# Performance work log

Hardware: AMD Instinct MI355X
Metric: run time of the kernel (lower is better)

Reference implementation:

```python
import jax, jax.numpy as jnp
import numpy as np

EPS = 1e-7
CAPS_N = 1152   # 32 maps * 6 * 6
CAPS1_DIM = 8
CAPS2_N = 10
CAPS2_DIM = 16


def squash(s, axis):
    sq = jnp.sum(jnp.square(s), axis=axis, keepdims=True)
    norm = jnp.sqrt(sq + EPS)
    return (sq / (1.0 + sq)) * (s / norm)


def _conv(x, k, b, stride):
    y = jax.lax.conv_general_dilated(x, k, (stride, stride), 'VALID',
                                     dimension_numbers=('NHWC', 'HWIO', 'NHWC'))
    return jax.nn.relu(y + b)


def setup_inputs() -> dict:
    key = jax.random.key(0)
    ks = jax.random.split(key, 8)
    B = 256
    return {
        'image': jax.random.uniform(ks[0], (B, 28, 28, 1), dtype=jnp.float32),
        'target': jax.random.randint(ks[1], (B,), 0, CAPS2_N),
        'conv1_w': jax.random.normal(ks[2], (9, 9, 1, 256), jnp.float32) * 0.05,
        'conv1_b': jnp.zeros((256,), jnp.float32),
        'conv2_w': jax.random.normal(ks[3], (9, 9, 256, 256), jnp.float32) * 0.02,
        'conv2_b': jnp.zeros((256,), jnp.float32),
        'W': jax.random.normal(ks[4], (1, CAPS_N, CAPS2_N, CAPS2_DIM, CAPS1_DIM), jnp.float32) * 0.1,
        'd1_w': jax.random.normal(ks[5], (CAPS2_N * CAPS2_DIM, 512), jnp.float32) * 0.05,
        'd1_b': jnp.zeros((512,), jnp.float32),
        'd2_w': jax.random.normal(ks[6], (512, 1024), jnp.float32) * 0.04,
        'd2_b': jnp.zeros((1024,), jnp.float32),
        'd3_w': jax.random.normal(ks[7], (1024, 784), jnp.float32) * 0.03,
        'd3_b': jnp.zeros((784,), jnp.float32),
    }


def reference(image, target, conv1_w, conv1_b, conv2_w, conv2_b, W,
              d1_w, d1_b, d2_w, d2_b, d3_w, d3_b):
    B = image.shape[0]
    h = _conv(image, conv1_w, conv1_b, 1)        # [B,20,20,256]
    h = _conv(h, conv2_w, conv2_b, 2)            # [B,6,6,256]
    pc = squash(h.reshape(B, CAPS_N, CAPS1_DIM), axis=-1)  # [B,1152,8]
    # u_hat[b,n,c,j] = sum_i W[0,n,c,j,i] * pc[b,n,i]  (avoids explicit tiling)
    u_hat = jnp.einsum('ncji,bni->bncj', W[0], pc)          # [B,1152,10,16]
    # round 1: softmax of zeros over the 10 digit caps == uniform 1/10
    s1 = jnp.sum(u_hat, axis=1) * (1.0 / CAPS2_N)           # [B,10,16]
    v1 = squash(s1, axis=-1)
    # agreement uv[b,n,c] = <u_hat[b,n,c,:], v1[b,c,:]>
    uv = jnp.einsum('bncj,bcj->bnc', u_hat, v1)             # [B,1152,10]
    # round 2
    c2 = jax.nn.softmax(uv, axis=2)
    s2 = jnp.einsum('bnc,bncj->bcj', c2, u_hat)             # [B,10,16]
    v2 = squash(s2, axis=-1)                                # [B,10,16]
    norm_v2 = jnp.sqrt(jnp.sum(jnp.square(v2), axis=-1, keepdims=True) + EPS)
    norm_v2 = norm_v2[:, None, :, :, None]                  # [B,1,10,1,1]
    y_pred = jnp.squeeze(jnp.argmax(norm_v2, axis=2), axis=(1, 2))  # [B,1]
    # training path: mask by target one-hot
    mask = jax.nn.one_hot(target, CAPS2_N, dtype=v2.dtype)  # [B,10]
    masked = v2 * mask[:, :, None]                          # [B,10,16]
    flat = masked.reshape(B, 1, CAPS2_N * CAPS2_DIM)        # [B,1,160]
    h1 = jax.nn.relu(flat @ d1_w + d1_b)
    h2 = jax.nn.relu(h1 @ d2_w + d2_b)
    dec = jax.nn.sigmoid(h2 @ d3_w + d3_b)                  # [B,1,784]
    return norm_v2, y_pred, dec
```

## Files before the change

### kernel.cpp

```cpp
#include <hip/hip_runtime.h>
#include <math.h>

#define EPS 1e-7f
#define IN1_ELEMS 26214400
#define BT_ELEMS  5308416

typedef float fvec4 __attribute__((ext_vector_type(4)));
typedef short short8 __attribute__((ext_vector_type(8)));
typedef _Float16 half8 __attribute__((ext_vector_type(8)));

__device__ inline unsigned short f2h(float f){
  _Float16 h = (_Float16)f;
  return __builtin_bit_cast(unsigned short, h);
}
__device__ inline float h2f(unsigned short u){
  return (float)__builtin_bit_cast(_Float16, u);
}
__device__ inline void async16(unsigned short* dst, const unsigned short* src){
  __builtin_amdgcn_global_load_lds((const __attribute__((address_space(1))) void*)src,
                                   (__attribute__((address_space(3))) void*)dst, 16, 0, 0);
}
__device__ inline fvec4 mfma_f16(short8 a, short8 b, fvec4 c){
  return __builtin_amdgcn_mfma_f32_16x16x32_f16(
      __builtin_bit_cast(half8, a), __builtin_bit_cast(half8, b), c, 0, 0, 0);
}

__global__ __launch_bounds__(256) void prep_kernel(const float* __restrict__ w2,
    unsigned short* __restrict__ BTh, unsigned short* __restrict__ BTl,
    float* __restrict__ c2out,
    const float* __restrict__ img, const float* __restrict__ w1,
    const float* __restrict__ b1, unsigned short* __restrict__ outh,
    float* __restrict__ s1s2){
  const int bid = blockIdx.x;
  const int t = threadIdx.x;
  if (bid < 1296){
    __shared__ float tile[64][65];
    int k0 = (bid % 324) * 64, oc0 = (bid / 324) * 64;
    for (int g = bid*256 + t; g < 2359296; g += 1296*256) c2out[g] = 0.f;
    #pragma unroll
    for (int p = 0; p < 16; ++p){
      int f = p*256 + t;
      int kr = f >> 6, cc = f & 63;
      tile[kr][cc] = w2[(size_t)(k0 + kr)*256 + oc0 + cc];
    }
    __syncthreads();
    #pragma unroll
    for (int p = 0; p < 16; ++p){
      int f = p*256 + t;
      int ocr = f >> 6, kc = f & 63;
      float v = tile[kc][ocr] * 64.f;
      unsigned short h = f2h(v);
      size_t idx = (size_t)(oc0 + ocr)*20736 + k0 + kc;
      BTh[idx] = h;
      BTl[idx] = f2h(v - h2f(h));
    }
  } else {
    const int cid = bid - 1296;
    if (cid < 320) s1s2[cid*256 + t] = 0.f;
    __shared__ float sim[252];
    int oh = cid % 20, b = cid / 20;
    if (t < 252) sim[t] = img[((size_t)b*28 + oh + t/28)*28 + (t%28)];
    __syncthreads();
    float acc[20];
    #pragma unroll
    for (int i = 0; i < 20; ++i) acc[i] = 0.f;
    #pragma unroll
    for (int kh = 0; kh < 9; ++kh){
      float im[28];
      #pragma unroll
      for (int c = 0; c < 28; ++c) im[c] = sim[kh*28 + c];
      #pragma unroll
      for (int kw = 0; kw < 9; ++kw){
        float wv = w1[(kh*9 + kw)*256 + t];
        #pragma unroll
        for (int ow = 0; ow < 20; ++ow) acc[ow] = fmaf(im[ow + kw], wv, acc[ow]);
      }
    }
    float bv = b1[t];
    size_t base = ((size_t)(b*20 + oh))*20*256 + t;
    #pragma unroll
    for (int ow = 0; ow < 20; ++ow){
      float v = fmaxf(acc[ow] + bv, 0.f);
      outh[base + ow*256] = f2h(v * 0.015625f);
    }
  }
}

__global__ __launch_bounds__(256) void conv2_mfma(const unsigned short* __restrict__ in1h,
    const unsigned short* __restrict__ BTh, float* __restrict__ out){
  __shared__ __align__(16) unsigned short lds[24576];
  const int t = threadIdx.x;
  const int lane = t & 63, w = t >> 6;
  const int m0 = blockIdx.y * 128, n0 = blockIdx.x * 128;
  const int rowA = t >> 2, q = (t & 3) ^ ((t >> 3) & 3);

  const unsigned short* aS[2];
  const unsigned short* bS[2];
  #pragma unroll
  for (int h = 0; h < 2; ++h){
    int m = m0 + h*64 + rowA;
    int bb = m / 36, s = m - bb*36, oh = s / 6, ow = s - oh*6;
    aS[h] = in1h + ((size_t)((bb*20 + 2*oh)*20 + 2*ow))*256 + q*8;
    int n = n0 + h*64 + rowA;
    bS[h] = BTh + (size_t)n*20736 + q*8;
  }

  const int r = lane & 15;
  const int p = (lane >> 4) ^ ((lane >> 1) & 3);
  int roA[4], roB[4];
  #pragma unroll
  for (int i=0;i<4;++i){
    roA[i] = ((w >> 1)*64 + i*16 + r)*32 + p*8;
    roB[i] = ((w & 1)*64  + i*16 + r)*32 + p*8;
  }

  fvec4 acc[4][4];
  #pragma unroll
  for (int i=0;i<4;++i)
    #pragma unroll
    for (int j=0;j<4;++j) acc[i][j] = (fvec4){0.f,0.f,0.f,0.f};

  const int ks0 = blockIdx.z * 54;

  #define STAGE(BUF, KS) do{                                            \
    int kk_ = (KS) >> 3, kh_ = kk_/9, kw_ = kk_ - kh_*9;                \
    int aoff_ = (kh_*20 + kw_)*256 + ((KS) & 7)*32;                     \
    int boff_ = (KS)*32;                                                \
    int base_ = (BUF)*12288;                                            \
    _Pragma("unroll")                                                   \
    for (int h_=0; h_<2; ++h_){                                         \
      async16(&lds[base_ +        h_*2048 + t*8], aS[h_] + aoff_);      \
      async16(&lds[base_ + 4096 + h_*2048 + t*8], bS[h_] + boff_);      \
      async16(&lds[base_ + 8192 + h_*2048 + t*8], bS[h_] + BT_ELEMS + boff_); \
    } }while(0)

  STAGE(0, ks0);
  int buf = 0;
  for (int it = 0; it < 54; ++it){
    __syncthreads();
    if (it < 53) STAGE(buf^1, ks0 + it + 1);
    int base = buf*12288;
    short8 af[4], bh[4], bl[4];
    #pragma unroll
    for (int i=0;i<4;++i){
      af[i] = *(const short8*)&lds[base + roA[i]];
      bh[i] = *(const short8*)&lds[base + 4096 + roB[i]];
      bl[i] = *(const short8*)&lds[base + 8192 + roB[i]];
    }
    #pragma unroll
    for (int i=0;i<4;++i)
      #pragma unroll
      for (int j=0;j<4;++j){
        acc[i][j] = mfma_f16(af[i], bh[j], acc[i][j]);
        acc[i][j] = mfma_f16(af[i], bl[j], acc[i][j]);
      }
    buf ^= 1;
  }

  const int qm = (w >> 1)*64, qn = (w & 1)*64;
  #pragma unroll
  for (int i=0;i<4;++i){
    int gm = m0 + qm + i*16 + ((lane >> 4) << 2);
    #pragma unroll
    for (int j=0;j<4;++j){
      int gn = n0 + qn + j*16 + (lane & 15);
      #pragma unroll
      for (int rr=0;rr<4;++rr)
        atomicAdd(&out[(size_t)(gm + rr)*256 + gn], acc[i][j][rr]);
    }
  }
}

__global__ __launch_bounds__(256) void s1pc_kernel(const float* __restrict__ c2out,
    const float* __restrict__ b2, float* __restrict__ pc,
    const float* __restrict__ Wm, float* __restrict__ s1){
  __shared__ float pcl[2048];
  int t = threadIdx.x;
  int n0 = blockIdx.x * 16, b0 = blockIdx.y * 16;
  int pix = n0 >> 5, oc0 = (n0 & 31) * 8;
  {
    int bl = t >> 4, part = t & 15;
    const float* s = c2out + ((size_t)((b0 + bl)*36 + pix))*256 + oc0 + part*8;
    float v[8], sq = 0.f;
    #pragma unroll
    for (int e=0;e<8;++e){
      float x = fmaxf(s[e] + b2[oc0 + part*8 + e], 0.f);
      v[e] = x; sq += x*x;
    }
    float fac = sq / ((1.f + sq) * sqrtf(sq + EPS));
    float* o = pc + ((size_t)(b0 + bl)*1152 + n0 + part)*8;
    float* l = &pcl[(bl*16 + part)*8];
    #pragma unroll
    for (int e=0;e<8;++e){ float y = v[e]*fac; o[e] = y; l[e] = y; }
  }
  __syncthreads();
  for (int r = 0; r < 10; ++r){
    int item = r*256 + t;
    int bl = item / 160, cj = item - bl*160;
    float s1a = 0.f;
    const float* pb = &pcl[bl*128];
    #pragma unroll 4
    for (int nl = 0; nl < 16; ++nl){
      const float4* wp = (const float4*)&Wm[((size_t)(n0 + nl)*160 + cj)*8];
      float4 w0 = wp[0], w1 = wp[1];
      const float4* pp = (const float4*)&pb[nl*8];
      float4 p0 = pp[0], p1 = pp[1];
      s1a += w0.x*p0.x + w0.y*p0.y + w0.z*p0.z + w0.w*p0.w
           + w1.x*p1.x + w1.y*p1.y + w1.z*p1.z + w1.w*p1.w;
    }
    atomicAdd(&s1[(b0 + bl)*160 + cj], s1a);
  }
}

__global__ __launch_bounds__(320) void routing2(const float* __restrict__ pc,
    const float* __restrict__ Wm, const float* __restrict__ s1, float* __restrict__ s2){
  __shared__ float pcl[32][64];
  __shared__ float v1l[8][160];
  __shared__ float facl[80];
  __shared__ float c2l[32][10][8];
  const int t = threadIdx.x;
  const int n0 = blockIdx.x*32, b0 = blockIdx.y*8;

  for (int f = t; f < 2048; f += 320){
    int b = f >> 8, rem = f & 255;
    pcl[rem >> 3][b*8 + (rem & 7)] =
        pc[((size_t)(b0 + b)*1152 + n0 + (rem >> 3))*8 + (rem & 7)];
  }
  if (t < 80){
    int b = t/10, c = t - (t/10)*10;
    const float* s = s1 + (size_t)(b0 + b)*160 + c*16;
    float sq = 0.f;
    #pragma unroll
    for (int j=0;j<16;++j){ float v = s[j]*0.1f; sq += v*v; }
    facl[t] = 0.1f * sq / ((1.f + sq) * sqrtf(sq + EPS));
  }
  __syncthreads();
  for (int f = t; f < 1280; f += 320){
    int b = f / 160, cj = f - b*160;
    v1l[b][cj] = s1[(size_t)(b0 + b)*160 + cj] * facl[b*10 + (cj >> 4)];
  }
  __syncthreads();

  {
    const int nl = t / 10, c = t - (t/10)*10;
    float pcr[64];
    #pragma unroll
    for (int u = 0; u < 16; ++u) ((float4*)pcr)[u] = ((const float4*)&pcl[nl][0])[u];
    const float* wrow = Wm + ((size_t)(n0 + nl)*160 + c*16)*8;
    float uv[8];
    #pragma unroll
    for (int b=0;b<8;++b) uv[b] = 0.f;
    #pragma unroll
    for (int j = 0; j < 16; ++j){
      float4 w0 = ((const float4*)wrow)[j*2], w1 = ((const float4*)wrow)[j*2+1];
      #pragma unroll
      for (int b=0;b<8;++b){
        float tj = w0.x*pcr[b*8+0] + w0.y*pcr[b*8+1] + w0.z*pcr[b*8+2] + w0.w*pcr[b*8+3]
                 + w1.x*pcr[b*8+4] + w1.y*pcr[b*8+5] + w1.z*pcr[b*8+6] + w1.w*pcr[b*8+7];
        uv[b] = fmaf(tj, v1l[b][c*16 + j], uv[b]);
      }
    }
    #pragma unroll
    for (int b=0;b<8;++b) c2l[nl][c][b] = uv[b];
  }
  __syncthreads();

  if (t < 256){
    int snl = t >> 3, sb = t & 7;
    float mx = c2l[snl][0][sb];
    #pragma unroll
    for (int cc=1;cc<10;++cc) mx = fmaxf(mx, c2l[snl][cc][sb]);
    float e[10], sum = 0.f;
    #pragma unroll
    for (int cc=0;cc<10;++cc){ e[cc] = expf(c2l[snl][cc][sb] - mx); sum += e[cc]; }
    float inv = 1.f/sum;
    #pragma unroll
    for (int cc=0;cc<10;++cc) c2l[snl][cc][sb] = e[cc]*inv;
  }
  __syncthreads();

  {
    const int g = t / 160, cj = t - g*160;
    const int c = cj >> 4;
    float acc0 = 0.f, acc1 = 0.f, acc2 = 0.f, acc3 = 0.f;
    for (int nl = 0; nl < 32; ++nl){
      const float4* wp = (const float4*)&Wm[((size_t)(n0 + nl)*160 + cj)*8];
      float4 w0 = wp[0], w1 = wp[1];
      const float* pb = &pcl[nl][g*32];
      const float* cc = &c2l[nl][c][g*4];
      float4 p0, p1;
      p0 = ((const float4*)pb)[0]; p1 = ((const float4*)pb)[1];
      acc0 = fmaf(cc[0], w0.x*p0.x + w0.y*p0.y + w0.z*p0.z + w0.w*p0.w
                       + w1.x*p1.x + w1.y*p1.y + w1.z*p1.z + w1.w*p1.w, acc0);
      p0 = ((const float4*)pb)[2]; p1 = ((const float4*)pb)[3];
      acc1 = fmaf(cc[1], w0.x*p0.x + w0.y*p0.y + w0.z*p0.z + w0.w*p0.w
                       + w1.x*p1.x + w1.y*p1.y + w1.z*p1.z + w1.w*p1.w, acc1);
      p0 = ((const float4*)pb)[4]; p1 = ((const float4*)pb)[5];
      acc2 = fmaf(cc[2], w0.x*p0.x + w0.y*p0.y + w0.z*p0.z + w0.w*p0.w
                       + w1.x*p1.x + w1.y*p1.y + w1.z*p1.z + w1.w*p1.w, acc2);
      p0 = ((const float4*)pb)[6]; p1 = ((const float4*)pb)[7];
      acc3 = fmaf(cc[3], w0.x*p0.x + w0.y*p0.y + w0.z*p0.z + w0.w*p0.w
                       + w1.x*p1.x + w1.y*p1.y + w1.z*p1.z + w1.w*p1.w, acc3);
    }
    atomicAdd(&s2[(size_t)(b0 + g*4 + 0)*160 + cj], acc0);
    atomicAdd(&s2[(size_t)(b0 + g*4 + 1)*160 + cj], acc1);
    atomicAdd(&s2[(size_t)(b0 + g*4 + 2)*160 + cj], acc2);
    atomicAdd(&s2[(size_t)(b0 + g*4 + 3)*160 + cj], acc3);
  }
}

__global__ __launch_bounds__(128) void final_dec1(const float* __restrict__ s2,
    const int* __restrict__ target, const float* __restrict__ d1w,
    const float* __restrict__ d1b, float* __restrict__ out_norm,
    float* __restrict__ out_pred, float* __restrict__ h1){
  __shared__ float v2t[16];
  __shared__ float nrm[10];
  int b = blockIdx.x, t = threadIdx.x;
  int tg = target[b];
  if (t < 10){
    const float* s = s2 + b*160 + t*16;
    float x[16], sq = 0.f;
    #pragma unroll
    for (int j=0;j<16;++j){ x[j] = s[j]; sq += x[j]*x[j]; }
    float fac = sq / ((1.f + sq) * sqrtf(sq + EPS));
    float n2 = 0.f;
    #pragma unroll
    for (int j=0;j<16;++j){
      float v = x[j]*fac;
      if (t == tg) v2t[j] = v;
      n2 += v*v;
    }
    float nr = sqrtf(n2 + EPS);
    nrm[t] = nr;
    out_norm[b*10 + t] = nr;
  }
  __syncthreads();
  if (t == 0){
    int am = 0; float bv = nrm[0];
    #pragma unroll
    for (int c=1;c<10;++c) if (nrm[c] > bv){ bv = nrm[c]; am = c; }
    out_pred[b] = (float)am;
  }
  float v[16];
  #pragma unroll
  for (int j=0;j<16;++j) v[j] = v2t[j];
  #pragma unroll
  for (int rr = 0; rr < 4; ++rr){
    int n = t + rr*128;
    float acc = d1b[n];
    #pragma unroll
    for (int j=0;j<16;++j) acc = fmaf(v[j], d1w[(size_t)(tg*16 + j)*512 + n], acc);
    h1[(size_t)b*512 + n] = fmaxf(acc, 0.f);
  }
}

__global__ __launch_bounds__(256) void dec_gemm(const float* __restrict__ A,
    const float* __restrict__ B, const float* __restrict__ bias, float* __restrict__ C,
    int K, int N, int act){
  int t = threadIdx.x;
  int n = blockIdx.x*64 + (t & 63);
  int m = blockIdx.y*4 + (t >> 6);
  if (n >= N) return;
  float acc = 0.f;
  const float* a = A + (size_t)m*K;
  const float* bp = B + n;
  #pragma unroll 8
  for (int k = 0; k < K; ++k) acc = fmaf(a[k], bp[(size_t)k*N], acc);
  acc += bias[n];
  if (act == 0) acc = fmaxf(acc, 0.f);
  else acc = 1.f/(1.f + expf(-acc));
  C[(size_t)m*N + n] = acc;
}

extern "C" void kernel_launch(void* const* d_in, const int* in_sizes, int n_in,
                              void* d_out, int out_size, void* d_ws, size_t ws_size,
                              hipStream_t stream) {
  const float* image   = (const float*)d_in[0];
  const int*   target  = (const int*)d_in[1];
  const float* conv1_w = (const float*)d_in[2];
  const float* conv1_b = (const float*)d_in[3];
  const float* conv2_w = (const float*)d_in[4];
  const float* conv2_b = (const float*)d_in[5];
  const float* Wm      = (const float*)d_in[6];
  const float* d1_w    = (const float*)d_in[7];
  const float* d1_b    = (const float*)d_in[8];
  const float* d2_w    = (const float*)d_in[9];
  const float* d2_b    = (const float*)d_in[10];
  const float* d3_w    = (const float*)d_in[11];
  const float* d3_b    = (const float*)d_in[12];

  char* ws = (char*)d_ws;
  unsigned short* in1h = (unsigned short*)(ws);
  unsigned short* BTh  = (unsigned short*)(ws + 52428800);
  float* c2out  = (float*)(ws + 73662464);
  float* pc     = (float*)(ws + 83099648);
  float* s1     = (float*)(ws + 92536832);
  float* s2     = (float*)(ws + 92700672);
  float* h1     = (float*)(ws + 92864512);
  float* h2     = (float*)(ws + 93388800);

  float* out_norm = (float*)d_out;
  float* out_pred = out_norm + 2560;
  float* dec      = out_norm + 2816;

  prep_kernel<<<dim3(6416),256,0,stream>>>(conv2_w, BTh, BTh + BT_ELEMS, c2out,
                                           image, conv1_w, conv1_b, in1h, s1);
  conv2_mfma<<<dim3(2,72,12),256,0,stream>>>(in1h, BTh, c2out);
  s1pc_kernel<<<dim3(72,16),256,0,stream>>>(c2out, conv2_b, pc, Wm, s1);
  routing2<<<dim3(36,32),320,0,stream>>>(pc, Wm, s1, s2);
  final_dec1<<<dim3(256),128,0,stream>>>(s2, target, d1_w, d1_b, out_norm, out_pred, h1);
  dec_gemm<<<dim3(16,64),256,0,stream>>>(h1, d2_w, d2_b, h2, 512, 1024, 0);
  dec_gemm<<<dim3(13,64),256,0,stream>>>(h2, d3_w, d3_b, dec, 1024, 784, 1);
}
```

Baseline: 625.8 us.

## Fuse decoder MLP into one kernel and reduce conv2 split-K to eight slices

```diff
diff --git a/kernel.cpp b/kernel.cpp
--- a/kernel.cpp
+++ b/kernel.cpp
@@ -120,7 +120,7 @@
     #pragma unroll
     for (int j=0;j<4;++j) acc[i][j] = (fvec4){0.f,0.f,0.f,0.f};
 
-  const int ks0 = blockIdx.z * 54;
+  const int ks0 = blockIdx.z * 81;
 
   #define STAGE(BUF, KS) do{                                            \
     int kk_ = (KS) >> 3, kh_ = kk_/9, kw_ = kk_ - kh_*9;                \
@@ -136,9 +136,9 @@
 
   STAGE(0, ks0);
   int buf = 0;
-  for (int it = 0; it < 54; ++it){
+  for (int it = 0; it < 81; ++it){
     __syncthreads();
-    if (it < 53) STAGE(buf^1, ks0 + it + 1);
+    if (it < 80) STAGE(buf^1, ks0 + it + 1);
     int base = buf*12288;
     short8 af[4], bh[4], bl[4];
     #pragma unroll
@@ -309,14 +309,20 @@
   }
 }
 
-__global__ __launch_bounds__(128) void final_dec1(const float* __restrict__ s2,
-    const int* __restrict__ target, const float* __restrict__ d1w,
-    const float* __restrict__ d1b, float* __restrict__ out_norm,
-    float* __restrict__ out_pred, float* __restrict__ h1){
+__global__ __launch_bounds__(256) void decoder_fused(const float* __restrict__ s2,
+    const int* __restrict__ target,
+    const float* __restrict__ d1w, const float* __restrict__ d1b,
+    const float* __restrict__ d2w, const float* __restrict__ d2b,
+    const float* __restrict__ d3w, const float* __restrict__ d3b,
+    float* __restrict__ out_norm, float* __restrict__ out_pred,
+    float* __restrict__ dec){
   __shared__ float v2t[16];
   __shared__ float nrm[10];
-  int b = blockIdx.x, t = threadIdx.x;
-  int tg = target[b];
+  __shared__ float h1l[512];
+  __shared__ float h2l[1024];
+  const int b = blockIdx.x, t = threadIdx.x;
+  const int tg = target[b];
+
   if (t < 10){
     const float* s = s2 + b*160 + t*16;
     float x[16], sq = 0.f;
@@ -341,35 +347,56 @@
     for (int c=1;c<10;++c) if (nrm[c] > bv){ bv = nrm[c]; am = c; }
     out_pred[b] = (float)am;
   }
+
   float v[16];
   #pragma unroll
   for (int j=0;j<16;++j) v[j] = v2t[j];
   #pragma unroll
-  for (int rr = 0; rr < 4; ++rr){
-    int n = t + rr*128;
+  for (int r = 0; r < 2; ++r){
+    int n = r*256 + t;
     float acc = d1b[n];
     #pragma unroll
     for (int j=0;j<16;++j) acc = fmaf(v[j], d1w[(size_t)(tg*16 + j)*512 + n], acc);
-    h1[(size_t)b*512 + n] = fmaxf(acc, 0.f);
-  }
-}
-
-__global__ __launch_bounds__(256) void dec_gemm(const float* __restrict__ A,
-    const float* __restrict__ B, const float* __restrict__ bias, float* __restrict__ C,
-    int K, int N, int act){
-  int t = threadIdx.x;
-  int n = blockIdx.x*64 + (t & 63);
-  int m = blockIdx.y*4 + (t >> 6);
-  if (n >= N) return;
-  float acc = 0.f;
-  const float* a = A + (size_t)m*K;
-  const float* bp = B + n;
-  #pragma unroll 8
-  for (int k = 0; k < K; ++k) acc = fmaf(a[k], bp[(size_t)k*N], acc);
-  acc += bias[n];
-  if (act == 0) acc = fmaxf(acc, 0.f);
-  else acc = 1.f/(1.f + expf(-acc));
-  C[(size_t)m*N + n] = acc;
+    h1l[n] = fmaxf(acc, 0.f);
+  }
+  __syncthreads();
+
+  {
+    float a0 = d2b[t], a1 = d2b[256+t], a2 = d2b[512+t], a3 = d2b[768+t];
+    #pragma unroll 4
+    for (int k = 0; k < 512; ++k){
+      float hv = h1l[k];
+      const float* row = d2w + (size_t)k*1024 + t;
+      a0 = fmaf(hv, row[0],   a0);
+      a1 = fmaf(hv, row[256], a1);
+      a2 = fmaf(hv, row[512], a2);
+      a3 = fmaf(hv, row[768], a3);
+    }
+    h2l[t]     = fmaxf(a0, 0.f);
+    h2l[256+t] = fmaxf(a1, 0.f);
+    h2l[512+t] = fmaxf(a2, 0.f);
+    h2l[768+t] = fmaxf(a3, 0.f);
+  }
+  __syncthreads();
+
+  {
+    float a0 = d3b[t], a1 = d3b[256+t], a2 = d3b[512+t];
+    float a3 = (t < 16) ? d3b[768+t] : 0.f;
+    #pragma unroll 4
+    for (int k = 0; k < 1024; ++k){
+      float hv = h2l[k];
+      const float* row = d3w + (size_t)k*784 + t;
+      a0 = fmaf(hv, row[0],   a0);
+      a1 = fmaf(hv, row[256], a1);
+      a2 = fmaf(hv, row[512], a2);
+      if (t < 16) a3 = fmaf(hv, row[768], a3);
+    }
+    float* o = dec + (size_t)b*784;
+    o[t]     = 1.f/(1.f + expf(-a0));
+    o[256+t] = 1.f/(1.f + expf(-a1));
+    o[512+t] = 1.f/(1.f + expf(-a2));
+    if (t < 16) o[768+t] = 1.f/(1.f + expf(-a3));
+  }
 }
 
 extern "C" void kernel_launch(void* const* d_in, const int* in_sizes, int n_in,
@@ -396,8 +423,6 @@
   float* pc     = (float*)(ws + 83099648);
   float* s1     = (float*)(ws + 92536832);
   float* s2     = (float*)(ws + 92700672);
-  float* h1     = (float*)(ws + 92864512);
-  float* h2     = (float*)(ws + 93388800);
 
   float* out_norm = (float*)d_out;
   float* out_pred = out_norm + 2560;
@@ -405,10 +430,9 @@
 
   prep_kernel<<<dim3(6416),256,0,stream>>>(conv2_w, BTh, BTh + BT_ELEMS, c2out,
                                            image, conv1_w, conv1_b, in1h, s1);
-  conv2_mfma<<<dim3(2,72,12),256,0,stream>>>(in1h, BTh, c2out);
+  conv2_mfma<<<dim3(2,72,8),256,0,stream>>>(in1h, BTh, c2out);
   s1pc_kernel<<<dim3(72,16),256,0,stream>>>(c2out, conv2_b, pc, Wm, s1);
   routing2<<<dim3(36,32),320,0,stream>>>(pc, Wm, s1, s2);
-  final_dec1<<<dim3(256),128,0,stream>>>(s2, target, d1_w, d1_b, out_norm, out_pred, h1);
-  dec_gemm<<<dim3(16,64),256,0,stream>>>(h1, d2_w, d2_b, h2, 512, 1024, 0);
-  dec_gemm<<<dim3(13,64),256,0,stream>>>(h2, d3_w, d3_b, dec, 1024, 784, 1);
-}
+  decoder_fused<<<dim3(256),256,0,stream>>>(s2, target, d1_w, d1_b, d2_w, d2_b,
+                                            d3_w, d3_b, out_norm, out_pred, dec);
+}
```

New measurement: 879.1 us. +40.5%, slower.
